# Optimization experiments

Hardware: AMD Instinct MI355X
Metric: run time of the kernel (lower is better)

Reference implementation:

```python
import jax, jax.numpy as jnp
import numpy as np

NUM_HEADS = 16
D_MODEL = 1024
HEAD_DIM = D_MODEL // NUM_HEADS
SCALE = 8.0 / HEAD_DIM  # use_mup=True
LN_EPS = 1e-5


def setup_inputs() -> dict:
    key = jax.random.key(0)
    ks = jax.random.split(key, 8)
    B, N, M = 2, 2048, 2048
    std = 1.0 / np.sqrt(D_MODEL)
    return {
        "x1": jax.random.normal(ks[0], (B, N, D_MODEL), jnp.float32),
        "x2": jax.random.normal(ks[1], (B, M, D_MODEL), jnp.float32),
        "Wq": jax.random.normal(ks[2], (D_MODEL, D_MODEL), jnp.float32) * std,
        "Wk": jax.random.normal(ks[3], (D_MODEL, D_MODEL), jnp.float32) * std,
        "Wv": jax.random.normal(ks[4], (D_MODEL, D_MODEL), jnp.float32) * std,
        "Wp": jax.random.normal(ks[5], (D_MODEL, D_MODEL), jnp.float32) * std,
        "bp": jnp.zeros((D_MODEL,), jnp.float32),
        "ln_g": jnp.ones((HEAD_DIM,), jnp.float32),
        "ln_b": jnp.zeros((HEAD_DIM,), jnp.float32),
    }


def _layernorm(x, g, b):
    # LayerNorm over last dim (head_dim), eps=1e-5, biased variance (torch default)
    mu = jnp.mean(x, axis=-1, keepdims=True)
    var = jnp.mean(jnp.square(x - mu), axis=-1, keepdims=True)
    return (x - mu) * jax.lax.rsqrt(var + LN_EPS) * g + b


def reference(x1, x2, Wq, Wk, Wv, Wp, bp, ln_g, ln_b):
    B, N, C = x1.shape
    M = x2.shape[1]
    H, D = NUM_HEADS, HEAD_DIM
    # torch Linear: y = x @ W.T  (no qkv bias); reshape to [B, H, L, D]
    q = (x1 @ Wq.T).reshape(B, N, H, D).transpose(0, 2, 1, 3)
    k = (x2 @ Wk.T).reshape(B, M, H, D).transpose(0, 2, 1, 3)
    v = (x2 @ Wv.T).reshape(B, M, H, D).transpose(0, 2, 1, 3)
    # per-head QK LayerNorm (shared params)
    q = _layernorm(q, ln_g, ln_b)
    k = _layernorm(k, ln_g, ln_b)
    q = q * SCALE
    attn = jnp.einsum("bhnd,bhmd->bhnm", q, k)
    attn = jax.nn.softmax(attn, axis=-1)  # causal=False, attn_drop=0
    out = jnp.einsum("bhnm,bhmd->bhnd", attn, v)
    out = out.transpose(0, 2, 1, 3).reshape(B, N, C)
    return out @ Wp.T + bp
```

## Files before the change

kernel.cpp:

```cpp
#include <hip/hip_runtime.h>

#define DEV static __device__ __forceinline__

using bf16x8 = __attribute__((ext_vector_type(8))) short;
using f32x4  = __attribute__((ext_vector_type(4))) float;
using f32x16 = __attribute__((ext_vector_type(16))) float;

#if __has_builtin(__builtin_amdgcn_exp2f)
#define EXP2(x) __builtin_amdgcn_exp2f(x)
#else
#define EXP2(x) exp2f(x)
#endif

DEV unsigned short f2bf(float f) {
  union { float f; unsigned u; } v; v.f = f;
  return (unsigned short)((v.u + 0x7fffu + ((v.u >> 16) & 1u)) >> 16);
}
DEV float bf2f(unsigned short b) {
  union { unsigned u; float f; } v; v.u = ((unsigned)b) << 16;
  return v.f;
}
DEV unsigned cvtpk(float lo, float hi) {
  unsigned r;
  asm("v_cvt_pk_bf16_f32 %0, %1, %2" : "=v"(r) : "v"(lo), "v"(hi));
  return r;
}
DEV void pl32swap(unsigned &a, unsigned &b) {
  asm("v_permlane32_swap_b32 %0, %1" : "+v"(a), "+v"(b));
}
DEV bf16x8 mk8(unsigned a, unsigned b, unsigned c, unsigned d) {
  union { unsigned u[4]; bf16x8 v; } t;
  t.u[0] = a; t.u[1] = b; t.u[2] = c; t.u[3] = d;
  return t.v;
}
DEV f32x4 mfma16(bf16x8 a, bf16x8 b, f32x4 c) {
  return __builtin_amdgcn_mfma_f32_16x16x32_bf16(a, b, c, 0, 0, 0);
}
DEV f32x16 mfma32(bf16x8 a, bf16x8 b, f32x16 c) {
  return __builtin_amdgcn_mfma_f32_32x32x16_bf16(a, b, c, 0, 0, 0);
}
DEV f32x16 zero16() {
  f32x16 z;
#pragma unroll
  for (int i = 0; i < 16; ++i) z[i] = 0.f;
  return z;
}

typedef const __attribute__((address_space(1))) unsigned int* gas1;
typedef __attribute__((address_space(3))) unsigned int* las3;
DEV void gl16(const void* g, void* l) {
  __builtin_amdgcn_global_load_lds((gas1)g, (las3)l, 16, 0, 0);
}

__global__ __launch_bounds__(256, 8)
void conv_bf16(const float* __restrict__ x1, const float* __restrict__ x2,
               const float* __restrict__ Wq, const float* __restrict__ Wk,
               const float* __restrict__ Wv, const float* __restrict__ Wp,
               unsigned short* __restrict__ o)
{
  size_t e = ((size_t)blockIdx.x * 256 + threadIdx.x) * 8;
  const float* s; size_t off;
  if (e < 4194304u)       { s = x1; off = e; }
  else if (e < 8388608u)  { s = x2; off = e - 4194304u; }
  else if (e < 9437184u)  { s = Wq; off = e - 8388608u; }
  else if (e < 10485760u) { s = Wk; off = e - 9437184u; }
  else if (e < 11534336u) { s = Wv; off = e - 10485760u; }
  else                    { s = Wp; off = e - 11534336u; }
  const float4* p = reinterpret_cast<const float4*>(s + off);
  float4 a = p[0], b = p[1];
  int4 r;
  r.x = (int)cvtpk(a.x, a.y); r.y = (int)cvtpk(a.z, a.w);
  r.z = (int)cvtpk(b.x, b.y); r.w = (int)cvtpk(b.z, b.w);
  *reinterpret_cast<int4*>(o + e) = r;
}

__global__ __launch_bounds__(256, 4)
void gemm_qkv_bf(const unsigned short* __restrict__ xb,
                 const float* __restrict__ lg, const float* __restrict__ lb,
                 unsigned short* __restrict__ qb, unsigned short* __restrict__ kb,
                 unsigned short* __restrict__ vtb)
{
  __shared__ short As[128 * 64];
  __shared__ short Bs[128 * 64];
  const int tid = threadIdx.x;
  const int l = tid & 63, w = tid >> 6;
  const int wr = w >> 1, wc = w & 1;
  const int z = blockIdx.z;
  const unsigned short* A = (z == 0) ? xb : (xb + 4194304);
  const unsigned short* W = xb + 8388608 + (size_t)z * 1048576;
  const int id = blockIdx.x + (blockIdx.y << 3);
  const int tl = ((id & 7) << 5) | (id >> 3);
  const int bx = tl & 7, by = tl >> 3;
  const int brow = by * 128, bcol = bx * 128;

  const f32x4 zero = {0.f, 0.f, 0.f, 0.f};
  f32x4 acc[4][4];
#pragma unroll
  for (int mi = 0; mi < 4; ++mi)
#pragma unroll
    for (int ni = 0; ni < 4; ++ni) acc[mi][ni] = zero;

  const int srow = w * 32 + (l >> 3);
  const int scol = (l & 7) * 8;

  for (int kt = 0; kt < 16; ++kt) {
    const unsigned short* ga = A + (size_t)(brow + srow) * 1024 + kt * 64 + scol;
    const unsigned short* gb = W + (size_t)(bcol + srow) * 1024 + kt * 64 + scol;
#pragma unroll
    for (int i = 0; i < 4; ++i) {
      gl16(ga + (size_t)i * 8 * 1024, &As[(w * 32 + i * 8) * 64]);
      gl16(gb + (size_t)i * 8 * 1024, &Bs[(w * 32 + i * 8) * 64]);
    }
    __syncthreads();
#pragma unroll
    for (int kk = 0; kk < 2; ++kk) {
      const int k0 = kk * 32 + ((l >> 4) << 3);
      bf16x8 af[4], bfr[4];
#pragma unroll
      for (int mi = 0; mi < 4; ++mi)
        af[mi] = *reinterpret_cast<const bf16x8*>(
            &As[((wr << 6) + (mi << 4) + (l & 15)) * 64 + k0]);
#pragma unroll
      for (int ni = 0; ni < 4; ++ni)
        bfr[ni] = *reinterpret_cast<const bf16x8*>(
            &Bs[((wc << 6) + (ni << 4) + (l & 15)) * 64 + k0]);
#pragma unroll
      for (int mi = 0; mi < 4; ++mi)
#pragma unroll
        for (int ni = 0; ni < 4; ++ni)
          acc[mi][ni] = mfma16(af[mi], bfr[ni], acc[mi][ni]);
    }
    __syncthreads();
  }

  if (z < 2) {
    unsigned short* dst = (z == 0) ? qb : kb;
    const float scl = (z == 0) ? 0.18033688011112042f : 1.0f;
    const int h = bx * 2 + wc;
    float gw4[4], bw4[4];
#pragma unroll
    for (int ni = 0; ni < 4; ++ni) {
      gw4[ni] = lg[ni * 16 + (l & 15)] * scl;
      bw4[ni] = lb[ni * 16 + (l & 15)] * scl;
    }
#pragma unroll
    for (int mi = 0; mi < 4; ++mi) {
      float ylo[4];
#pragma unroll
      for (int r = 0; r < 4; ++r) {
        float v0 = acc[mi][0][r], v1 = acc[mi][1][r];
        float v2 = acc[mi][2][r], v3 = acc[mi][3][r];
        float s  = (v0 + v1) + (v2 + v3);
        float s2 = (v0 * v0 + v1 * v1) + (v2 * v2 + v3 * v3);
#pragma unroll
        for (int off = 1; off < 16; off <<= 1) {
          s  += __shfl_xor(s, off);
          s2 += __shfl_xor(s2, off);
        }
        float mean = s * (1.f / 64.f);
        float var  = s2 * (1.f / 64.f) - mean * mean;
        float rstd = rsqrtf(var + 1e-5f);
        float y[4];
        y[0] = (v0 - mean) * rstd * gw4[0] + bw4[0];
        y[1] = (v1 - mean) * rstd * gw4[1] + bw4[1];
        y[2] = (v2 - mean) * rstd * gw4[2] + bw4[2];
        y[3] = (v3 - mean) * rstd * gw4[3] + bw4[3];
        if (!(r & 1)) {
          ylo[0] = y[0]; ylo[1] = y[1]; ylo[2] = y[2]; ylo[3] = y[3];
        } else {
          int rowg0 = brow + (wr << 6) + (mi << 4) + ((l >> 4) << 2) + r - 1;
          int b = rowg0 >> 11, n = rowg0 & 2047;
          unsigned short* base =
              dst + (((size_t)(b * 16 + h) << 11) + n) * 64 + (l & 15);
#pragma unroll
          for (int ni = 0; ni < 4; ++ni) {
            unsigned u = cvtpk(ylo[ni], y[ni]);
            base[ni * 16]      = (unsigned short)(u & 0xffffu);
            base[ni * 16 + 64] = (unsigned short)(u >> 16);
          }
        }
      }
    }
  } else {
    const int bb = brow >> 11;
    const int nblk = brow & 2047;
#pragma unroll
    for (int mi = 0; mi < 4; ++mi)
#pragma unroll
      for (int ni = 0; ni < 4; ++ni) {
        int n0 = nblk + (wr << 6) + (mi << 4) + ((l >> 4) << 2);
        int colg = bcol + (wc << 6) + (ni << 4) + (l & 15);
        int h = colg >> 6, d = colg & 63;
        unsigned u0 = cvtpk(acc[mi][ni][0], acc[mi][ni][1]);
        unsigned u1 = cvtpk(acc[mi][ni][2], acc[mi][ni][3]);
        int2 u; u.x = (int)u0; u.y = (int)u1;
        *reinterpret_cast<int2*>(
            &vtb[((size_t)(bb * 16 + h) * 64 + d) * 2048 + n0]) = u;
      }
  }
}

__global__ __launch_bounds__(128, 2)
void attn_fwd(const unsigned short* __restrict__ Q,
              const unsigned short* __restrict__ K,
              const unsigned short* __restrict__ Vt,
              unsigned short* __restrict__ pnum,
              float* __restrict__ plsum)
{
  __shared__ short Ks[2][64 * 64];
  __shared__ short Vs[2][64 * 64];
  const int tid = threadIdx.x, w = tid >> 6, l = tid & 63;
  const int lo5 = l & 31, hi = l >> 5;
  const int bh = blockIdx.y;
  const int half = blockIdx.z;
  const int tbase = half * 16;
  const int qbase = blockIdx.x * 128 + w * 64;
  const unsigned short* Qg = Q + ((size_t)bh * 2048 + qbase) * 64;
  const unsigned short* Kg = K + (size_t)bh * 2048 * 64;
  const unsigned short* Vg = Vt + (size_t)bh * 64 * 2048;

  bf16x8 qfA[4], qfB[4];
#pragma unroll
  for (int ks = 0; ks < 4; ++ks) {
    qfA[ks] = *reinterpret_cast<const bf16x8*>(Qg + lo5 * 64 + ks * 16 + hi * 8);
    qfB[ks] = *reinterpret_cast<const bf16x8*>(Qg + (32 + lo5) * 64 + ks * 16 + hi * 8);
  }
  const bf16x8 ones = mk8(0x3F803F80u, 0x3F803F80u, 0x3F803F80u, 0x3F803F80u);

  f32x16 oc0a = zero16(), oc1a = zero16(), lsa = zero16();
  f32x16 oc0b = zero16(), oc1b = zero16(), lsb = zero16();

  const int srow = tid >> 3;
  const int scs = (((tid & 7) ^ (srow & 7)) * 8);

  const unsigned short* kp = Kg + (size_t)tbase * 4096 + srow * 64 + scs;
  const unsigned short* vp = Vg + (size_t)tbase * 64 + (size_t)srow * 2048 + scs;
  short* kd0 = &Ks[0][w * 512]; short* kd1 = &Ks[1][w * 512];
  short* vd0 = &Vs[0][w * 512]; short* vd1 = &Vs[1][w * 512];

#define STAGEKV(KD, VD)                                                        \
  gl16(kp,         (KD));                                                      \
  gl16(kp + 1024,  (KD) + 1024);                                               \
  gl16(kp + 2048,  (KD) + 2048);                                               \
  gl16(kp + 3072,  (KD) + 3072);                                               \
  gl16(vp,         (VD));                                                      \
  gl16(vp + 32768, (VD) + 1024);                                               \
  gl16(vp + 65536, (VD) + 2048);                                               \
  gl16(vp + 98304, (VD) + 3072);                                               \
  kp += 4096; vp += 64

  STAGEKV(kd0, vd0);
  __syncthreads();

  for (int it = 0; it < 16; ++it) {
    const int cur = it & 1;
    const short* Kc = Ks[cur];
    const short* Vc = Vs[cur];

    if (it < 15) {
      if (cur == 0) { STAGEKV(kd1, vd1); }
      else          { STAGEKV(kd0, vd0); }
    }

    f32x16 s0a = zero16(), s1a = zero16(), s0b = zero16(), s1b = zero16();
    __builtin_amdgcn_s_setprio(1);
#pragma unroll
    for (int ks = 0; ks < 4; ++ks) {
      const int colc = (16 * ks + 8 * hi) ^ ((lo5 & 7) << 3);
      bf16x8 k0 = *reinterpret_cast<const bf16x8*>(&Kc[(lo5 << 6) + colc]);
      bf16x8 k1 = *reinterpret_cast<const bf16x8*>(&Kc[((32 + lo5) << 6) + colc]);
      s0a = mfma32(k0, qfA[ks], s0a);
      s1a = mfma32(k1, qfA[ks], s1a);
      s0b = mfma32(k0, qfB[ks], s0b);
      s1b = mfma32(k1, qfB[ks], s1b);
    }
    __builtin_amdgcn_s_setprio(0);

    auto pvpair = [&](const f32x16& sa, const f32x16& sb, int jbase) {
      float pA[16], pB[16];
#pragma unroll
      for (int r = 0; r < 16; ++r) { pA[r] = EXP2(sa[r]); pB[r] = EXP2(sb[r]); }
#pragma unroll
      for (int f = 0; f < 2; ++f) {
        unsigned xA  = cvtpk(pA[8 * f + 0], pA[8 * f + 1]);
        unsigned zA  = cvtpk(pA[8 * f + 2], pA[8 * f + 3]);
        unsigned yA  = cvtpk(pA[8 * f + 4], pA[8 * f + 5]);
        unsigned wA  = cvtpk(pA[8 * f + 6], pA[8 * f + 7]);
        pl32swap(xA, yA);
        pl32swap(zA, wA);
        bf16x8 paA = mk8(xA, zA, yA, wA);
        unsigned xB  = cvtpk(pB[8 * f + 0], pB[8 * f + 1]);
        unsigned zB  = cvtpk(pB[8 * f + 2], pB[8 * f + 3]);
        unsigned yB  = cvtpk(pB[8 * f + 4], pB[8 * f + 5]);
        unsigned wB  = cvtpk(pB[8 * f + 6], pB[8 * f + 7]);
        pl32swap(xB, yB);
        pl32swap(zB, wB);
        bf16x8 paB = mk8(xB, zB, yB, wB);
        const int colc = (jbase + 16 * f + 8 * hi);
        bf16x8 v0 = *reinterpret_cast<const bf16x8*>(
            &Vc[(lo5 << 6) + (colc ^ ((lo5 & 7) << 3))]);
        bf16x8 v1 = *reinterpret_cast<const bf16x8*>(
            &Vc[((32 + lo5) << 6) + (colc ^ ((lo5 & 7) << 3))]);
        __builtin_amdgcn_s_setprio(1);
        oc0a = mfma32(paA, v0, oc0a);
        oc1a = mfma32(paA, v1, oc1a);
        lsa  = mfma32(paA, ones, lsa);
        oc0b = mfma32(paB, v0, oc0b);
        oc1b = mfma32(paB, v1, oc1b);
        lsb  = mfma32(paB, ones, lsb);
        __builtin_amdgcn_s_setprio(0);
      }
    };
    pvpair(s0a, s0b, 0);
    pvpair(s1a, s1b, 32);

    __syncthreads();
  }
#undef STAGEKV

  unsigned short* Pn = pnum + ((size_t)(half * 32 + bh) * 2048 + qbase) * 64;
#pragma unroll
  for (int r = 0; r < 16; ++r) {
    int qrow = (r & 3) + 8 * (r >> 2) + 4 * hi;
    Pn[qrow * 64 + lo5]             = f2bf(oc0a[r]);
    Pn[qrow * 64 + 32 + lo5]        = f2bf(oc1a[r]);
    Pn[(32 + qrow) * 64 + lo5]      = f2bf(oc0b[r]);
    Pn[(32 + qrow) * 64 + 32 + lo5] = f2bf(oc1b[r]);
  }
  if (lo5 == 0) {
    float* Pl = plsum + (size_t)(half * 32 + bh) * 2048 + qbase;
#pragma unroll
    for (int r = 0; r < 16; ++r) {
      int qrow = (r & 3) + 8 * (r >> 2) + 4 * hi;
      Pl[qrow]      = lsa[r];
      Pl[32 + qrow] = lsb[r];
    }
  }
}

__global__ __launch_bounds__(256, 8)
void attn_combine(const unsigned short* __restrict__ pnum,
                  const float* __restrict__ plsum,
                  unsigned short* __restrict__ obuf)
{
  const int t = blockIdx.x * 256 + threadIdx.x;
  const int bh = t >> 14;
  const int rem = t & 16383;
  const int q = rem >> 3, dblk = rem & 7;
  const size_t i0 = (((size_t)bh * 2048) + q) * 64 + dblk * 8;
  const size_t i1 = i0 + (size_t)32 * 2048 * 64;
  ushort4 a0 = *reinterpret_cast<const ushort4*>(pnum + i0);
  ushort4 a1 = *reinterpret_cast<const ushort4*>(pnum + i0 + 4);
  ushort4 b0 = *reinterpret_cast<const ushort4*>(pnum + i1);
  ushort4 b1 = *reinterpret_cast<const ushort4*>(pnum + i1 + 4);
  float ls = plsum[bh * 2048 + q] + plsum[65536 + bh * 2048 + q];
  float inv = 1.f / ls;
  ushort4 o0, o1;
  o0.x = f2bf((bf2f(a0.x) + bf2f(b0.x)) * inv);
  o0.y = f2bf((bf2f(a0.y) + bf2f(b0.y)) * inv);
  o0.z = f2bf((bf2f(a0.z) + bf2f(b0.z)) * inv);
  o0.w = f2bf((bf2f(a0.w) + bf2f(b0.w)) * inv);
  o1.x = f2bf((bf2f(a1.x) + bf2f(b1.x)) * inv);
  o1.y = f2bf((bf2f(a1.y) + bf2f(b1.y)) * inv);
  o1.z = f2bf((bf2f(a1.z) + bf2f(b1.z)) * inv);
  o1.w = f2bf((bf2f(a1.w) + bf2f(b1.w)) * inv);
  unsigned short* dst = obuf + ((size_t)(bh >> 4) * 2048 + q) * 1024 +
                        (bh & 15) * 64 + dblk * 8;
  *reinterpret_cast<ushort4*>(dst) = o0;
  *reinterpret_cast<ushort4*>(dst + 4) = o1;
}

__global__ __launch_bounds__(256, 4)
void gemm_out_bf(const unsigned short* __restrict__ ob,
                 const unsigned short* __restrict__ wpb,
                 const float* __restrict__ bp, float* __restrict__ out)
{
  __shared__ short As[128 * 64];
  __shared__ short Bs[128 * 64];
  const int tid = threadIdx.x;
  const int l = tid & 63, w = tid >> 6;
  const int wr = w >> 1, wc = w & 1;
  const int id = blockIdx.x + (blockIdx.y << 3);
  const int tl = ((id & 7) << 5) | (id >> 3);
  const int brow = (tl >> 3) * 128, bcol = (tl & 7) * 128;

  const f32x4 zero = {0.f, 0.f, 0.f, 0.f};
  f32x4 acc[4][4];
#pragma unroll
  for (int mi = 0; mi < 4; ++mi)
#pragma unroll
    for (int ni = 0; ni < 4; ++ni) acc[mi][ni] = zero;

  const int srow = w * 32 + (l >> 3);
  const int scol = (l & 7) * 8;

  for (int kt = 0; kt < 16; ++kt) {
    const unsigned short* ga = ob + (size_t)(brow + srow) * 1024 + kt * 64 + scol;
    const unsigned short* gb = wpb + (size_t)(bcol + srow) * 1024 + kt * 64 + scol;
#pragma unroll
    for (int i = 0; i < 4; ++i) {
      gl16(ga + (size_t)i * 8 * 1024, &As[(w * 32 + i * 8) * 64]);
      gl16(gb + (size_t)i * 8 * 1024, &Bs[(w * 32 + i * 8) * 64]);
    }
    __syncthreads();
#pragma unroll
    for (int kk = 0; kk < 2; ++kk) {
      const int k0 = kk * 32 + ((l >> 4) << 3);
      bf16x8 af[4], bfr[4];
#pragma unroll
      for (int mi = 0; mi < 4; ++mi)
        af[mi] = *reinterpret_cast<const bf16x8*>(
            &As[((wr << 6) + (mi << 4) + (l & 15)) * 64 + k0]);
#pragma unroll
      for (int ni = 0; ni < 4; ++ni)
        bfr[ni] = *reinterpret_cast<const bf16x8*>(
            &Bs[((wc << 6) + (ni << 4) + (l & 15)) * 64 + k0]);
#pragma unroll
      for (int mi = 0; mi < 4; ++mi)
#pragma unroll
        for (int ni = 0; ni < 4; ++ni)
          acc[mi][ni] = mfma16(af[mi], bfr[ni], acc[mi][ni]);
    }
    __syncthreads();
  }

  float bias[4];
#pragma unroll
  for (int ni = 0; ni < 4; ++ni)
    bias[ni] = bp[bcol + (wc << 6) + (ni << 4) + (l & 15)];
#pragma unroll
  for (int mi = 0; mi < 4; ++mi)
#pragma unroll
    for (int ni = 0; ni < 4; ++ni)
#pragma unroll
      for (int r = 0; r < 4; ++r) {
        int rowg = brow + (wr << 6) + (mi << 4) + ((l >> 4) << 2) + r;
        int colg = bcol + (wc << 6) + (ni << 4) + (l & 15);
        out[(size_t)rowg * 1024 + colg] = acc[mi][ni][r] + bias[ni];
      }
}

extern "C" void kernel_launch(void* const* d_in, const int* in_sizes, int n_in,
                              void* d_out, int out_size, void* d_ws, size_t ws_size,
                              hipStream_t stream)
{
  const float* x1 = (const float*)d_in[0];
  const float* x2 = (const float*)d_in[1];
  const float* Wq = (const float*)d_in[2];
  const float* Wk = (const float*)d_in[3];
  const float* Wv = (const float*)d_in[4];
  const float* Wp = (const float*)d_in[5];
  const float* bp = (const float*)d_in[6];
  const float* lg = (const float*)d_in[7];
  const float* lb = (const float*)d_in[8];

  char* wsb = (char*)d_ws;
  unsigned short* xb   = (unsigned short*)wsb;
  unsigned short* qb   = (unsigned short*)(wsb + 25165824);
  unsigned short* kb   = qb + 4194304;
  unsigned short* vtb  = kb + 4194304;
  unsigned short* obuf = vtb + 4194304;
  unsigned short* pnum = obuf + 4194304;
  float* plsum = (float*)(wsb + 75497472);
  float* out = (float*)d_out;

  conv_bf16<<<6144, 256, 0, stream>>>(x1, x2, Wq, Wk, Wv, Wp, xb);
  gemm_qkv_bf<<<dim3(8, 32, 3), 256, 0, stream>>>(xb, lg, lb, qb, kb, vtb);
  attn_fwd<<<dim3(16, 32, 2), 128, 0, stream>>>(qb, kb, vtb, pnum, plsum);
  attn_combine<<<2048, 256, 0, stream>>>(pnum, plsum, obuf);
  gemm_out_bf<<<dim3(8, 32), 256, 0, stream>>>(obuf,
      xb + 11534336, bp, out);
}
```

Measured before the change: 124.5 us.

## Split attention KV range into four partitions and combine four partials

The attention kernel's key/value split goes from two halves to four quarters. Each block now runs 8 KV tiles instead of 16, and the grid's z dimension doubles so there are more blocks to spread across the GPU. The combine kernel now sums four partial numerators and four partial row sums. The partial row sums move to the start of the workspace, which frees space for the larger partial buffers. In exchange, more partial output is written and read back, and the shorter loop has less work to hide its pipeline prologue behind.

```diff
diff --git a/kernel.cpp b/kernel.cpp
--- a/kernel.cpp
+++ b/kernel.cpp
@@ -213,7 +213,7 @@
   const int lo5 = l & 31, hi = l >> 5;
   const int bh = blockIdx.y;
   const int half = blockIdx.z;
-  const int tbase = half * 16;
+  const int tbase = half * 8;
   const int qbase = blockIdx.x * 128 + w * 64;
   const unsigned short* Qg = Q + ((size_t)bh * 2048 + qbase) * 64;
   const unsigned short* Kg = K + (size_t)bh * 2048 * 64;
@@ -252,12 +252,12 @@
   STAGEKV(kd0, vd0);
   __syncthreads();
 
-  for (int it = 0; it < 16; ++it) {
+  for (int it = 0; it < 8; ++it) {
     const int cur = it & 1;
     const short* Kc = Ks[cur];
     const short* Vc = Vs[cur];
 
-    if (it < 15) {
+    if (it < 7) {
       if (cur == 0) { STAGEKV(kd1, vd1); }
       else          { STAGEKV(kd0, vd0); }
     }
@@ -348,22 +348,27 @@
   const int rem = t & 16383;
   const int q = rem >> 3, dblk = rem & 7;
   const size_t i0 = (((size_t)bh * 2048) + q) * 64 + dblk * 8;
-  const size_t i1 = i0 + (size_t)32 * 2048 * 64;
-  ushort4 a0 = *reinterpret_cast<const ushort4*>(pnum + i0);
-  ushort4 a1 = *reinterpret_cast<const ushort4*>(pnum + i0 + 4);
-  ushort4 b0 = *reinterpret_cast<const ushort4*>(pnum + i1);
-  ushort4 b1 = *reinterpret_cast<const ushort4*>(pnum + i1 + 4);
-  float ls = plsum[bh * 2048 + q] + plsum[65536 + bh * 2048 + q];
+  const size_t STR = (size_t)32 * 2048 * 64;
+  float acc[8];
+#pragma unroll
+  for (int e = 0; e < 8; ++e) acc[e] = 0.f;
+#pragma unroll
+  for (int h = 0; h < 4; ++h) {
+    ushort4 a0 = *reinterpret_cast<const ushort4*>(pnum + i0 + h * STR);
+    ushort4 a1 = *reinterpret_cast<const ushort4*>(pnum + i0 + h * STR + 4);
+    acc[0] += bf2f(a0.x); acc[1] += bf2f(a0.y);
+    acc[2] += bf2f(a0.z); acc[3] += bf2f(a0.w);
+    acc[4] += bf2f(a1.x); acc[5] += bf2f(a1.y);
+    acc[6] += bf2f(a1.z); acc[7] += bf2f(a1.w);
+  }
+  float ls = (plsum[bh * 2048 + q]           + plsum[65536 + bh * 2048 + q]) +
+             (plsum[131072 + bh * 2048 + q]  + plsum[196608 + bh * 2048 + q]);
   float inv = 1.f / ls;
   ushort4 o0, o1;
-  o0.x = f2bf((bf2f(a0.x) + bf2f(b0.x)) * inv);
-  o0.y = f2bf((bf2f(a0.y) + bf2f(b0.y)) * inv);
-  o0.z = f2bf((bf2f(a0.z) + bf2f(b0.z)) * inv);
-  o0.w = f2bf((bf2f(a0.w) + bf2f(b0.w)) * inv);
-  o1.x = f2bf((bf2f(a1.x) + bf2f(b1.x)) * inv);
-  o1.y = f2bf((bf2f(a1.y) + bf2f(b1.y)) * inv);
-  o1.z = f2bf((bf2f(a1.z) + bf2f(b1.z)) * inv);
-  o1.w = f2bf((bf2f(a1.w) + bf2f(b1.w)) * inv);
+  o0.x = f2bf(acc[0] * inv); o0.y = f2bf(acc[1] * inv);
+  o0.z = f2bf(acc[2] * inv); o0.w = f2bf(acc[3] * inv);
+  o1.x = f2bf(acc[4] * inv); o1.y = f2bf(acc[5] * inv);
+  o1.z = f2bf(acc[6] * inv); o1.w = f2bf(acc[7] * inv);
   unsigned short* dst = obuf + ((size_t)(bh >> 4) * 2048 + q) * 1024 +
                         (bh & 15) * 64 + dblk * 8;
   *reinterpret_cast<ushort4*>(dst) = o0;
@@ -461,12 +466,12 @@
   unsigned short* vtb  = kb + 4194304;
   unsigned short* obuf = vtb + 4194304;
   unsigned short* pnum = obuf + 4194304;
-  float* plsum = (float*)(wsb + 75497472);
+  float* plsum = (float*)wsb;
   float* out = (float*)d_out;
 
   conv_bf16<<<6144, 256, 0, stream>>>(x1, x2, Wq, Wk, Wv, Wp, xb);
   gemm_qkv_bf<<<dim3(8, 32, 3), 256, 0, stream>>>(xb, lg, lb, qb, kb, vtb);
-  attn_fwd<<<dim3(16, 32, 2), 128, 0, stream>>>(qb, kb, vtb, pnum, plsum);
+  attn_fwd<<<dim3(16, 32, 4), 128, 0, stream>>>(qb, kb, vtb, pnum, plsum);
   attn_combine<<<2048, 256, 0, stream>>>(pnum, plsum, obuf);
   gemm_out_bf<<<dim3(8, 32), 256, 0, stream>>>(obuf,
       xb + 11534336, bp, out);
```

Measured after the change: 132.7 us. 1.07x slower.
